# Kernel optimization log

Measured on AMD Instinct MI355X. Metric: run time of the kernel, lower is better.

The kernel has to match this reference:

```python
import jax, jax.numpy as jnp
import numpy as np
from functools import partial

NUM_ITERS = 3
NUM_CAPS = 8      # primary capsule count
NUM_CLASSES = 10
OUT_CH = 16       # digit capsule dim
INPUT_SIZE = 32 * 6 * 6  # 1152 primary capsule units per capsule map


def squash(s, axis=-1):
    # faithful to non_linear_squashing: s * (||s||^2/(1+||s||^2)) / (||s||+1e-10)
    norm_sqr = jnp.sum(s * s, axis=axis, keepdims=True)
    scale = jnp.sqrt(norm_sqr) + 1e-10
    mag = norm_sqr / (1.0 + norm_sqr)
    return s * mag / scale


def conv2d(x, w, b, stride):
    y = jax.lax.conv_general_dilated(
        x, w, window_strides=(stride, stride), padding='VALID',
        dimension_numbers=('NCHW', 'OIHW', 'NCHW'))
    return y + b[None, :, None, None]


def setup_inputs() -> dict:
    key = jax.random.key(0)
    ks = jax.random.split(key, 6)
    B = 256
    x = jax.random.normal(ks[0], (B, 1, 28, 28), dtype=jnp.float32)
    conv_w = jax.random.normal(ks[1], (256, 1, 9, 9), dtype=jnp.float32) * 0.05
    conv_b = jax.random.normal(ks[2], (256,), dtype=jnp.float32) * 0.05
    # 8 primary capsule conv units (256->32 each) fused into one 256->256 conv
    prim_w = jax.random.normal(ks[3], (NUM_CAPS * 32, 256, 9, 9), dtype=jnp.float32) * 0.02
    prim_b = jax.random.normal(ks[4], (NUM_CAPS * 32,), dtype=jnp.float32) * 0.02
    # digit routing weights (input_size, num_classes, out_channels, num_capsules)
    digit_w = jax.random.normal(ks[5], (INPUT_SIZE, NUM_CLASSES, OUT_CH, NUM_CAPS), dtype=jnp.float32)
    return {'x': x, 'conv_w': conv_w, 'conv_b': conv_b,
            'prim_w': prim_w, 'prim_b': prim_b, 'digit_w': digit_w}


def reference(x, conv_w, conv_b, prim_w, prim_b, digit_w):
    B = x.shape[0]
    # conv stack: 1->256 k9 s1 + ReLU  (28 -> 20); pool is MaxPool2d(1,1) = identity
    h = jax.nn.relu(conv2d(x, conv_w, conv_b, stride=1))  # (B,256,20,20)
    # primary capsules: 8 convs 256->32 k9 s2, no activation (nl_activation=False)
    p = conv2d(h, prim_w, prim_b, stride=2)               # (B,256,6,6)
    u = p.reshape(B, NUM_CAPS, -1)                        # (B,8,1152)
    u = squash(u, axis=-1)
    # digit layer with dynamic routing
    # u_i: (B, IS, 8);  u_j_i[b,i,c,o] = sum_k W[i,c,o,k] * u_i[b,i,k]
    u_i = jnp.transpose(u, (0, 2, 1))                     # (B,1152,8)
    u_j_i = jnp.einsum('icok,bik->bico', digit_w, u_i)    # (B,1152,10,16)
    b_ij = jnp.zeros((INPUT_SIZE, NUM_CLASSES), dtype=x.dtype)
    out = None
    for _ in range(NUM_ITERS):
        c_ij = jax.nn.softmax(b_ij, axis=0)               # softmax over input capsules (dim=1 in torch)
        s_j = jnp.einsum('ic,bico->bco', c_ij, u_j_i)     # (B,10,16)
        # original squashes (B,1,C,16,1) along dim=2 == the CLASS axis
        out = squash(s_j, axis=1)                         # (B,10,16)
        # agreement: mean over batch of <u_j_i, v_j>
        u_v = jnp.einsum('bico,bco->ic', u_j_i, out) / B  # (1152,10)
        b_ij = b_ij + u_v
    # torch returns out.squeeze(1) with shape (B, C, 16, 1)
    return out[..., None]
```

## Files before the change

kernel.cpp:

```cpp
#include <hip/hip_runtime.h>
#include <cstdint>
#include <cstddef>


typedef __attribute__((ext_vector_type(8))) short short8;
typedef __attribute__((ext_vector_type(4))) float f32x4;

#define PHALF 2359296

__device__ __forceinline__ unsigned short f2bf_rn(float x) {
    unsigned u = __float_as_uint(x);
    unsigned r = (u + 0x7fffu + ((u >> 16) & 1u)) >> 16;
    return (unsigned short)r;
}

__global__ void k_makew(const float* __restrict__ w2,
                        unsigned short* __restrict__ wt) {
    __shared__ float lw[20736];
    int ocg = blockIdx.x, icg = blockIdx.y, t = threadIdx.x;
    for (int idx = t; idx < 20736; idx += 256) {
        int row = idx / 81, k = idx % 81;
        int oc_l = row >> 5, ic_l = row & 31;
        lw[idx] = w2[((size_t)(ocg * 8 + oc_l) * 256 + icg * 32 + ic_l) * 81 + k];
    }
    __syncthreads();
    for (int idx = t; idx < 2592; idx += 256) {
        int k = idx >> 5;
        int r = idx & 31;
        int oc_l = r >> 2, sl = r & 3;
        unsigned short hi8[8];
        #pragma unroll
        for (int j = 0; j < 8; j++)
            hi8[j] = f2bf_rn(lw[(oc_l * 32 + sl * 8 + j) * 81 + k]);
        size_t o = ((size_t)(k * 256 + ocg * 8 + oc_l)) * 256 + icg * 32 + sl * 8;
        *(uint4*)&wt[o] = *(uint4*)hi8;
    }
}

__global__ void k_conv1(const float* __restrict__ x, const float* __restrict__ cw,
                        const float* __restrict__ cb,
                        unsigned short* __restrict__ h) {
    __shared__ float img[784];
    __shared__ float wsm[32 * 81];
    int b = blockIdx.x, ocg = blockIdx.y, t = threadIdx.x;
    for (int idx = t; idx < 784; idx += 256) img[idx] = x[b * 784 + idx];
    for (int idx = t; idx < 2592; idx += 256) wsm[idx] = cw[ocg * 2592 + idx];
    __syncthreads();
    int oc_l = t & 31, g = t >> 5;
    int oc = ocg * 32 + oc_l;
    float bias = cb[oc];
    const float* wp = &wsm[oc_l * 81];
    for (int q = g; q < 100; q += 8) {
        int py = q / 5, qx = (q % 5) * 4;
        float a0 = bias, a1 = bias, a2 = bias, a3 = bias;
        #pragma unroll
        for (int ky = 0; ky < 9; ky++) {
            const float* ir = &img[(py + ky) * 28 + qx];
            float r[12];
            #pragma unroll
            for (int j = 0; j < 12; j++) r[j] = ir[j];
            #pragma unroll
            for (int kx = 0; kx < 9; kx++) {
                float w = wp[ky * 9 + kx];
                a0 += r[kx] * w; a1 += r[kx + 1] * w;
                a2 += r[kx + 2] * w; a3 += r[kx + 3] * w;
            }
        }
        float v[4] = { fmaxf(a0, 0.f), fmaxf(a1, 0.f), fmaxf(a2, 0.f), fmaxf(a3, 0.f) };
        size_t base = ((size_t)b * 400 + py * 20 + qx) * 256 + oc;
        #pragma unroll
        for (int j = 0; j < 4; j++)
            h[base + (size_t)j * 256] = f2bf_rn(v[j]);
    }
}

__global__ __launch_bounds__(256) void k_conv2m(
    const unsigned short* __restrict__ h,
    const unsigned short* __restrict__ wt,
    float* __restrict__ pp)
{
    __shared__ unsigned short smem[24576];
    const int t = threadIdx.x;
    const int w = t >> 6, l = t & 63;
    const int mb = blockIdx.x, nb = blockIdx.y, z = blockIdx.z;

    const unsigned short* src;
    int nld, sbase;
    unsigned rowbase[16];
    if (w < 2) {
        src = h; nld = 16; sbase = w * 8192;
        #pragma unroll
        for (int ld = 0; ld < 16; ld++) {
            int row = ld * 8 + (l >> 3);
            int c = l & 7;
            int g = c ^ (row & 7);
            int P = mb * 128 + row;
            int b = P / 36, o = P % 36;
            int oy = o / 6, ox = o % 6;
            rowbase[ld] = (unsigned)((b * 400 + oy * 40 + ox * 2) * 256 + z * 128 + w * 64 + g * 8);
        }
    } else {
        int hh = w - 2;
        src = wt; nld = 8; sbase = 16384 + hh * 4096;
        #pragma unroll
        for (int ld = 0; ld < 8; ld++) {
            int oc = ld * 8 + (l >> 3);
            int c = l & 7;
            int g = c ^ (oc & 7);
            rowbase[ld] = (unsigned)((nb * 64 + oc) * 256 + z * 128 + hh * 64 + g * 8);
        }
    }

    const int wm = w & 1, wn = w >> 1;
    const int lane16 = l & 15, q = l >> 4;

    f32x4 acc[4][2] = {};

    for (int ky = 0; ky < 9; ky++) {
        for (int kx = 0; kx < 9; kx++) {
            const unsigned kofs = (w < 2) ? (unsigned)((ky * 20 + kx) * 256)
                                          : (unsigned)((ky * 9 + kx) * 65536);
            __syncthreads();
            for (int ld = 0; ld < nld; ld++) {
                __builtin_amdgcn_global_load_lds(
                    (const __attribute__((address_space(1))) unsigned int*)(const void*)(src + rowbase[ld] + kofs),
                    (__attribute__((address_space(3))) unsigned int*)(void*)(smem + sbase + ld * 512),
                    16, 0, 0);
            }
            __syncthreads();
            #pragma unroll
            for (int hh = 0; hh < 2; hh++) {
                #pragma unroll
                for (int ic2 = 0; ic2 < 2; ic2++) {
                    short8 a[4], b[2];
                    #pragma unroll
                    for (int mt = 0; mt < 4; mt++) {
                        int pixL = wm * 64 + mt * 16 + lane16;
                        int ps = (ic2 * 4 + q) ^ (pixL & 7);
                        a[mt] = *(const short8*)(smem + hh * 8192 + pixL * 64 + ps * 8);
                    }
                    #pragma unroll
                    for (int nt = 0; nt < 2; nt++) {
                        int ocL = wn * 32 + nt * 16 + lane16;
                        int ps = (ic2 * 4 + q) ^ (ocL & 7);
                        b[nt] = *(const short8*)(smem + 16384 + hh * 4096 + ocL * 64 + ps * 8);
                    }
                    #pragma unroll
                    for (int mt = 0; mt < 4; mt++)
                        #pragma unroll
                        for (int nt = 0; nt < 2; nt++)
                            acc[mt][nt] = __builtin_amdgcn_mfma_f32_16x16x32_bf16(a[mt], b[nt], acc[mt][nt], 0, 0, 0);
                }
            }
        }
    }

    float* pout = pp + (size_t)z * PHALF;
    #pragma unroll
    for (int mt = 0; mt < 4; mt++) {
        int pixG = mb * 128 + wm * 64 + mt * 16 + q * 4;
        int b = pixG / 36, p36 = pixG % 36;
        #pragma unroll
        for (int nt = 0; nt < 2; nt++) {
            int oc = nb * 64 + wn * 32 + nt * 16 + lane16;
            f32x4 v = acc[mt][nt];
            *(f32x4*)&pp[0] ;
            *(f32x4*)&pout[((size_t)(b * 256 + oc)) * 36 + p36] = v;
        }
    }
}

__global__ void k_squash1(const float* __restrict__ pp, const float* __restrict__ prim_b,
                          float* __restrict__ U) {
    __shared__ float red[4];
    int b = blockIdx.x >> 3, cap = blockIdx.x & 7;
    int t = threadIdx.x;
    const float* pa = pp + ((size_t)b * 256 + cap * 32) * 36;
    const float* pc = pa + PHALF;
    float v[5];
    float ss = 0.f;
    #pragma unroll
    for (int j = 0; j < 5; j++) {
        int idx = t + j * 256;
        if (idx < 1152) {
            int ch_l = idx / 36;
            float val = pa[idx] + pc[idx] + prim_b[cap * 32 + ch_l];
            v[j] = val; ss += val * val;
        } else v[j] = 0.f;
    }
    for (int off = 32; off; off >>= 1) ss += __shfl_down(ss, off);
    if ((t & 63) == 0) red[t >> 6] = ss;
    __syncthreads();
    float n2 = red[0] + red[1] + red[2] + red[3];
    float f = (n2 / (1.0f + n2)) / (sqrtf(n2) + 1e-10f);
    #pragma unroll
    for (int j = 0; j < 5; j++) {
        int idx = t + j * 256;
        if (idx < 1152) U[(size_t)b * 9216 + idx * 8 + cap] = v[j] * f;
    }
}

__global__ void k_dwt2(const float* __restrict__ dw, float* __restrict__ dwT2) {
    int co = blockIdx.x, t = threadIdx.x;
    int c = co >> 4, o = co & 15;
    const float* base = dw + c * 128 + o * 8;
    float* out = dwT2 + (size_t)co * 9216;
    for (int idx = t; idx < 9216; idx += 256) {
        int i = idx >> 3, k = idx & 7;
        out[idx] = base[(size_t)i * 1280 + k];
    }
}

__global__ void k_ut(const float* __restrict__ U, float* __restrict__ UT) {
    __shared__ float tl[64][65];
    int ikb = blockIdx.x, bb = blockIdx.y, t = threadIdx.x;
    for (int idx = t; idx < 1024; idx += 256) {
        int row = idx >> 4, c4 = idx & 15;
        float4 v = *(const float4*)&U[(size_t)(bb * 64 + row) * 9216 + ikb * 64 + c4 * 4];
        tl[c4 * 4 + 0][row] = v.x;
        tl[c4 * 4 + 1][row] = v.y;
        tl[c4 * 4 + 2][row] = v.z;
        tl[c4 * 4 + 3][row] = v.w;
    }
    __syncthreads();
    for (int idx = t; idx < 1024; idx += 256) {
        int row = idx >> 4, c4 = idx & 15;
        float4 v = make_float4(tl[row][c4 * 4 + 0], tl[row][c4 * 4 + 1],
                               tl[row][c4 * 4 + 2], tl[row][c4 * 4 + 3]);
        *(float4*)&UT[(size_t)(ikb * 64 + row) * 256 + bb * 64 + c4 * 4] = v;
    }
}

__global__ void k_softmax(const float* __restrict__ bij, float* __restrict__ csm) {
    __shared__ float red[4];
    int c = blockIdx.x, t = threadIdx.x;
    float vals[5];
    float mx = -1e30f;
    #pragma unroll
    for (int j = 0; j < 5; j++) {
        int i = t + j * 256;
        vals[j] = (i < 1152) ? bij[i * 10 + c] : -1e30f;
        mx = fmaxf(mx, vals[j]);
    }
    for (int off = 32; off; off >>= 1) mx = fmaxf(mx, __shfl_down(mx, off));
    if ((t & 63) == 0) red[t >> 6] = mx;
    __syncthreads();
    mx = fmaxf(fmaxf(red[0], red[1]), fmaxf(red[2], red[3]));
    __syncthreads();
    float s = 0.f;
    #pragma unroll
    for (int j = 0; j < 5; j++) {
        int i = t + j * 256;
        vals[j] = (i < 1152) ? expf(vals[j] - mx) : 0.f;
        s += vals[j];
    }
    for (int off = 32; off; off >>= 1) s += __shfl_down(s, off);
    if ((t & 63) == 0) red[t >> 6] = s;
    __syncthreads();
    s = red[0] + red[1] + red[2] + red[3];
    float inv = 1.0f / s;
    #pragma unroll
    for (int j = 0; j < 5; j++) {
        int i = t + j * 256;
        if (i < 1152) csm[i * 10 + c] = vals[j] * inv;
    }
}

__global__ __launch_bounds__(256) void k_gemm1(const float* __restrict__ U,
                                               const float* __restrict__ dwT2,
                                               const float* __restrict__ csm,
                                               float* __restrict__ part,
                                               int uniform) {
    __shared__ float Us[32 * 36];
    __shared__ float WsT[5120];
    __shared__ float cl[360];
    int mb = blockIdx.x, kc = blockIdx.y, t = threadIdx.x;
    int tc = t & 15, tb = t >> 4;
    if (!uniform)
        for (int idx = t; idx < 360; idx += 256) cl[idx] = csm[kc * 360 + idx];
    const float uscale = 1.0f / 1152.0f;
    float acc[2][10] = {};
    for (int ks = 0; ks < 9; ks++) {
        __syncthreads();
        {
            int bb = t >> 3, k4 = t & 7;
            *(float4*)&Us[bb * 36 + k4 * 4] =
                *(const float4*)&U[(size_t)(mb * 32 + bb) * 9216 + kc * 288 + ks * 32 + k4 * 4];
        }
        #pragma unroll
        for (int pass = 0; pass < 5; pass++) {
            int s = t + pass * 256;
            int co = s >> 3, p = s & 7;
            int kq = p ^ (co & 7);
            int ikl = ks * 32 + kq * 4;
            float4 v = *(const float4*)&dwT2[(size_t)co * 9216 + kc * 288 + ikl];
            float sc = uniform ? uscale : cl[(ikl >> 3) * 10 + (co >> 4)];
            v.x *= sc; v.y *= sc; v.z *= sc; v.w *= sc;
            *(float4*)&WsT[s * 4] = v;
        }
        __syncthreads();
        float a0[32], a1[32];
        #pragma unroll
        for (int kq = 0; kq < 8; kq++) {
            float4 v0 = *(const float4*)&Us[(tb * 2) * 36 + kq * 4];
            float4 v1 = *(const float4*)&Us[(tb * 2 + 1) * 36 + kq * 4];
            a0[kq * 4 + 0] = v0.x; a0[kq * 4 + 1] = v0.y; a0[kq * 4 + 2] = v0.z; a0[kq * 4 + 3] = v0.w;
            a1[kq * 4 + 0] = v1.x; a1[kq * 4 + 1] = v1.y; a1[kq * 4 + 2] = v1.z; a1[kq * 4 + 3] = v1.w;
        }
        #pragma unroll
        for (int j = 0; j < 10; j++) {
            int co = tc + 16 * j;
            int cx = co & 7, cbase = co * 32;
            #pragma unroll
            for (int kq = 0; kq < 8; kq++) {
                float4 wv = *(const float4*)&WsT[cbase + ((kq ^ cx) << 2)];
                acc[0][j] += a0[kq * 4 + 0] * wv.x; acc[0][j] += a0[kq * 4 + 1] * wv.y;
                acc[0][j] += a0[kq * 4 + 2] * wv.z; acc[0][j] += a0[kq * 4 + 3] * wv.w;
                acc[1][j] += a1[kq * 4 + 0] * wv.x; acc[1][j] += a1[kq * 4 + 1] * wv.y;
                acc[1][j] += a1[kq * 4 + 2] * wv.z; acc[1][j] += a1[kq * 4 + 3] * wv.w;
            }
        }
    }
    #pragma unroll
    for (int r = 0; r < 2; r++)
        #pragma unroll
        for (int j = 0; j < 10; j++)
            part[(size_t)kc * 40960 + (mb * 32 + tb * 2 + r) * 160 + tc + 16 * j] = acc[r][j];
}

__global__ void k_redsq(const float* __restrict__ part, float* __restrict__ out,
                        float* __restrict__ outT, int writeT) {
    __shared__ float sl[160];
    __shared__ float n2s[16];
    int b = blockIdx.x, t = threadIdx.x;
    float s = 0.f;
    if (t < 160) {
        for (int kc = 0; kc < 32; kc++) s += part[(size_t)kc * 40960 + b * 160 + t];
        sl[t] = s;
    }
    __syncthreads();
    if (t < 16) {
        float n2 = 0.f;
        #pragma unroll
        for (int c = 0; c < 10; c++) { float v = sl[c * 16 + t]; n2 += v * v; }
        n2s[t] = n2;
    }
    __syncthreads();
    if (t < 160) {
        float n2 = n2s[t & 15];
        float f = (n2 / (1.0f + n2)) / (sqrtf(n2) + 1e-10f);
        float r = s * f;
        out[(size_t)b * 160 + t] = r;
        if (writeT) outT[(size_t)t * 256 + b] = r;
    }
}

__global__ __launch_bounds__(256) void k_g2uv(const float* __restrict__ UT,
                                              const float* __restrict__ outTg,
                                              const float* __restrict__ dw,
                                              float* __restrict__ bij) {
    __shared__ float UsT[1024];
    __shared__ float OsT[5120];
    __shared__ float dwl[5120];
    __shared__ float sb[320];
    int blk = blockIdx.x, t = threadIdx.x;
    int tc = t & 15, tm = t >> 4;
    for (int idx = t; idx < 5120; idx += 256)
        dwl[idx] = dw[(size_t)blk * 5120 + idx];
    float acc[2][10] = {};
    for (int bs = 0; bs < 256; bs += 32) {
        __syncthreads();
        {
            int m = t >> 3, p = t & 7;
            int kq = p ^ (m & 7);
            *(float4*)&UsT[t * 4] =
                *(const float4*)&UT[(size_t)(blk * 32 + m) * 256 + bs + kq * 4];
        }
        #pragma unroll
        for (int pass = 0; pass < 5; pass++) {
            int s = t + pass * 256;
            int co = s >> 3, p = s & 7;
            int kq = p ^ (co & 7);
            *(float4*)&OsT[s * 4] =
                *(const float4*)&outTg[(size_t)co * 256 + bs + kq * 4];
        }
        __syncthreads();
        float a0[32], a1[32];
        int m0 = tm * 2, m1 = tm * 2 + 1;
        #pragma unroll
        for (int kq = 0; kq < 8; kq++) {
            float4 v0 = *(const float4*)&UsT[m0 * 32 + ((kq ^ (m0 & 7)) << 2)];
            float4 v1 = *(const float4*)&UsT[m1 * 32 + ((kq ^ (m1 & 7)) << 2)];
            a0[kq * 4 + 0] = v0.x; a0[kq * 4 + 1] = v0.y; a0[kq * 4 + 2] = v0.z; a0[kq * 4 + 3] = v0.w;
            a1[kq * 4 + 0] = v1.x; a1[kq * 4 + 1] = v1.y; a1[kq * 4 + 2] = v1.z; a1[kq * 4 + 3] = v1.w;
        }
        #pragma unroll
        for (int j = 0; j < 10; j++) {
            int co = tc + 16 * j;
            int cx = co & 7, cbase = co * 32;
            #pragma unroll
            for (int kq = 0; kq < 8; kq++) {
                float4 wv = *(const float4*)&OsT[cbase + ((kq ^ cx) << 2)];
                acc[0][j] += a0[kq * 4 + 0] * wv.x; acc[0][j] += a0[kq * 4 + 1] * wv.y;
                acc[0][j] += a0[kq * 4 + 2] * wv.z; acc[0][j] += a0[kq * 4 + 3] * wv.w;
                acc[1][j] += a1[kq * 4 + 0] * wv.x; acc[1][j] += a1[kq * 4 + 1] * wv.y;
                acc[1][j] += a1[kq * 4 + 2] * wv.z; acc[1][j] += a1[kq * 4 + 3] * wv.w;
            }
        }
    }
    #pragma unroll
    for (int r = 0; r < 2; r++) {
        int ik_l = tm * 2 + r;
        int i_l = ik_l >> 3, k = ik_l & 7;
        #pragma unroll
        for (int j = 0; j < 10; j++) {
            float v = acc[r][j] * dwl[i_l * 1280 + (j * 16 + tc) * 8 + k];
            v += __shfl_down(v, 8, 16);
            v += __shfl_down(v, 4, 16);
            v += __shfl_down(v, 2, 16);
            v += __shfl_down(v, 1, 16);
            if (tc == 0) sb[ik_l * 10 + j] = v;
        }
    }
    __syncthreads();
    if (t < 40) {
        int i_l = t / 10, c = t % 10;
        float s = 0.f;
        #pragma unroll
        for (int kk = 0; kk < 8; kk++) s += sb[(i_l * 8 + kk) * 10 + c];
        size_t o = (size_t)(blk * 4 + i_l) * 10 + c;
        bij[o] += s * (1.0f / 256.0f);
    }
}

extern "C" void kernel_launch(void* const* d_in, const int* in_sizes, int n_in,
                              void* d_out, int out_size, void* d_ws, size_t ws_size,
                              hipStream_t stream) {
    const float* x      = (const float*)d_in[0];
    const float* conv_w = (const float*)d_in[1];
    const float* conv_b = (const float*)d_in[2];
    const float* prim_w = (const float*)d_in[3];
    const float* prim_b = (const float*)d_in[4];
    const float* dw     = (const float*)d_in[5];

    char* wsb = (char*)d_ws;
    unsigned short* h  = (unsigned short*)(wsb);
    unsigned short* wt = (unsigned short*)(wsb + 52428800);
    float* pp   = (float*)(wsb + 63045632);
    float* U    = (float*)(wsb + 81920000);
    float* dwT2 = (float*)(wsb + 91357184);
    float* part = (float*)(wsb + 97255424);
    float* csm  = (float*)(wsb + 102498304);
    float* bij  = (float*)(wsb + 102544384);
    float* outT = (float*)(wsb + 102590464);
    float* outw = (float*)(wsb + 102754304);
    float* UT   = (float*)(wsb + 102918144);

    k_makew<<<dim3(32, 8), 256, 0, stream>>>(prim_w, wt);
    k_conv1<<<dim3(256, 8), 256, 0, stream>>>(x, conv_w, conv_b, h);
    k_dwt2<<<160, 256, 0, stream>>>(dw, dwT2);
    k_conv2m<<<dim3(72, 4, 2), 256, 0, stream>>>(h, wt, pp);
    k_squash1<<<2048, 256, 0, stream>>>(pp, prim_b, U);
    k_ut<<<dim3(144, 4), 256, 0, stream>>>(U, UT);
    hipMemsetAsync(bij, 0, 11520 * sizeof(float), stream);

    k_gemm1<<<dim3(8, 32), 256, 0, stream>>>(U, dwT2, csm, part, 1);
    k_redsq<<<256, 256, 0, stream>>>(part, outw, outT, 1);
    k_g2uv<<<288, 256, 0, stream>>>(UT, outT, dw, bij);
    k_softmax<<<10, 256, 0, stream>>>(bij, csm);
    k_gemm1<<<dim3(8, 32), 256, 0, stream>>>(U, dwT2, csm, part, 0);
    k_redsq<<<256, 256, 0, stream>>>(part, outw, outT, 1);
    k_g2uv<<<288, 256, 0, stream>>>(UT, outT, dw, bij);
    k_softmax<<<10, 256, 0, stream>>>(bij, csm);
    k_gemm1<<<dim3(8, 32), 256, 0, stream>>>(U, dwT2, csm, part, 0);
    k_redsq<<<256, 256, 0, stream>>>(part, (float*)d_out, outT, 0);
}
```

Measured before the change: 508.6 us.

## Retile primary-capsule conv into 96x128 tiles with four-way split-K partials

The primary conv GEMM changes from 128x64 tiles with split over two channel halves to 96x128 tiles. Work is split four ways: two channel halves times two ranges of kernel positions. Each block now loads 64 input channels per stage into a smaller shared-memory buffer and declares launch bounds for higher occupancy. Four partial outputs are written to workspace regions that alias later buffers (dwT2, UT), so k_dwt2 is moved after the squash kernel that sums the four partials. The change aims for better MFMA reuse per loaded tile and more blocks in flight, at the cost of twice as many barrier-separated load stages and extra partial-sum traffic.

Result: faster. 490.7 us (-3.5%).

```diff
diff --git a/kernel.cpp b/kernel.cpp
--- a/kernel.cpp
+++ b/kernel.cpp
@@ -74,52 +74,57 @@
     }
 }
 
-__global__ __launch_bounds__(256) void k_conv2m(
+__global__ __launch_bounds__(256, 4) void k_conv2m(
     const unsigned short* __restrict__ h,
     const unsigned short* __restrict__ wt,
-    float* __restrict__ pp)
+    float* __restrict__ p0, float* __restrict__ p1,
+    float* __restrict__ p2, float* __restrict__ p3)
 {
-    __shared__ unsigned short smem[24576];
+    __shared__ unsigned short smem[14336];
     const int t = threadIdx.x;
     const int w = t >> 6, l = t & 63;
-    const int mb = blockIdx.x, nb = blockIdx.y, z = blockIdx.z;
+    const int mb = blockIdx.x, nb = blockIdx.y, zz = blockIdx.z;
+    const int half = zz >> 1, seg = zz & 1;
 
     const unsigned short* src;
     int nld, sbase;
-    unsigned rowbase[16];
+    unsigned rowbase[8];
     if (w < 2) {
-        src = h; nld = 16; sbase = w * 8192;
-        #pragma unroll
-        for (int ld = 0; ld < 16; ld++) {
-            int row = ld * 8 + (l >> 3);
+        src = h; nld = 6; sbase = w * 3072;
+        #pragma unroll
+        for (int ld = 0; ld < 6; ld++) {
+            int row = w * 48 + ld * 8 + (l >> 3);
             int c = l & 7;
             int g = c ^ (row & 7);
-            int P = mb * 128 + row;
+            int P = mb * 96 + row;
             int b = P / 36, o = P % 36;
             int oy = o / 6, ox = o % 6;
-            rowbase[ld] = (unsigned)((b * 400 + oy * 40 + ox * 2) * 256 + z * 128 + w * 64 + g * 8);
+            rowbase[ld] = (unsigned)((b * 400 + oy * 40 + ox * 2) * 256 + half * 128 + g * 8);
         }
     } else {
-        int hh = w - 2;
-        src = wt; nld = 8; sbase = 16384 + hh * 4096;
+        src = wt; nld = 8; sbase = 6144 + (w - 2) * 4096;
         #pragma unroll
         for (int ld = 0; ld < 8; ld++) {
-            int oc = ld * 8 + (l >> 3);
+            int oc = (w - 2) * 64 + ld * 8 + (l >> 3);
             int c = l & 7;
             int g = c ^ (oc & 7);
-            rowbase[ld] = (unsigned)((nb * 64 + oc) * 256 + z * 128 + hh * 64 + g * 8);
+            rowbase[ld] = (unsigned)((nb * 128 + oc) * 256 + half * 128 + g * 8);
         }
     }
 
     const int wm = w & 1, wn = w >> 1;
     const int lane16 = l & 15, q = l >> 4;
 
-    f32x4 acc[4][2] = {};
-
-    for (int ky = 0; ky < 9; ky++) {
-        for (int kx = 0; kx < 9; kx++) {
-            const unsigned kofs = (w < 2) ? (unsigned)((ky * 20 + kx) * 256)
-                                          : (unsigned)((ky * 9 + kx) * 65536);
+    f32x4 acc[3][4] = {};
+
+    const int pos0 = seg ? 41 : 0;
+    const int pos1 = seg ? 81 : 41;
+    for (int pos = pos0; pos < pos1; ++pos) {
+        const int ky = pos / 9, kx = pos - ky * 9;
+        const unsigned kbase = (w < 2) ? (unsigned)((ky * 20 + kx) * 256)
+                                       : (unsigned)(pos * 65536);
+        for (int icc = 0; icc < 2; ++icc) {
+            const unsigned kofs = kbase + icc * 64;
             __syncthreads();
             for (int ld = 0; ld < nld; ld++) {
                 __builtin_amdgcn_global_load_lds(
@@ -129,54 +134,53 @@
             }
             __syncthreads();
             #pragma unroll
-            for (int hh = 0; hh < 2; hh++) {
+            for (int ic2 = 0; ic2 < 2; ic2++) {
+                short8 a[3], b[4];
                 #pragma unroll
-                for (int ic2 = 0; ic2 < 2; ic2++) {
-                    short8 a[4], b[2];
+                for (int mt = 0; mt < 3; mt++) {
+                    int pixL = wm * 48 + mt * 16 + lane16;
+                    int ps = (ic2 * 4 + q) ^ (pixL & 7);
+                    a[mt] = *(const short8*)(smem + pixL * 64 + ps * 8);
+                }
+                #pragma unroll
+                for (int nt = 0; nt < 4; nt++) {
+                    int ocL = wn * 64 + nt * 16 + lane16;
+                    int ps = (ic2 * 4 + q) ^ (ocL & 7);
+                    b[nt] = *(const short8*)(smem + 6144 + ocL * 64 + ps * 8);
+                }
+                #pragma unroll
+                for (int mt = 0; mt < 3; mt++)
                     #pragma unroll
-                    for (int mt = 0; mt < 4; mt++) {
-                        int pixL = wm * 64 + mt * 16 + lane16;
-                        int ps = (ic2 * 4 + q) ^ (pixL & 7);
-                        a[mt] = *(const short8*)(smem + hh * 8192 + pixL * 64 + ps * 8);
-                    }
-                    #pragma unroll
-                    for (int nt = 0; nt < 2; nt++) {
-                        int ocL = wn * 32 + nt * 16 + lane16;
-                        int ps = (ic2 * 4 + q) ^ (ocL & 7);
-                        b[nt] = *(const short8*)(smem + 16384 + hh * 4096 + ocL * 64 + ps * 8);
-                    }
-                    #pragma unroll
-                    for (int mt = 0; mt < 4; mt++)
-                        #pragma unroll
-                        for (int nt = 0; nt < 2; nt++)
-                            acc[mt][nt] = __builtin_amdgcn_mfma_f32_16x16x32_bf16(a[mt], b[nt], acc[mt][nt], 0, 0, 0);
-                }
+                    for (int nt = 0; nt < 4; nt++)
+                        acc[mt][nt] = __builtin_amdgcn_mfma_f32_16x16x32_bf16(a[mt], b[nt], acc[mt][nt], 0, 0, 0);
             }
         }
     }
 
-    float* pout = pp + (size_t)z * PHALF;
-    #pragma unroll
-    for (int mt = 0; mt < 4; mt++) {
-        int pixG = mb * 128 + wm * 64 + mt * 16 + q * 4;
+    float* pout = (zz == 0) ? p0 : (zz == 1) ? p1 : (zz == 2) ? p2 : p3;
+    #pragma unroll
+    for (int mt = 0; mt < 3; mt++) {
+        int pixG = mb * 96 + wm * 48 + mt * 16 + q * 4;
         int b = pixG / 36, p36 = pixG % 36;
         #pragma unroll
-        for (int nt = 0; nt < 2; nt++) {
-            int oc = nb * 64 + wn * 32 + nt * 16 + lane16;
-            f32x4 v = acc[mt][nt];
-            *(f32x4*)&pp[0] ;
-            *(f32x4*)&pout[((size_t)(b * 256 + oc)) * 36 + p36] = v;
-        }
-    }
-}
-
-__global__ void k_squash1(const float* __restrict__ pp, const float* __restrict__ prim_b,
-                          float* __restrict__ U) {
+        for (int nt = 0; nt < 4; nt++) {
+            int oc = nb * 128 + wn * 64 + nt * 16 + lane16;
+            *(f32x4*)&pout[((size_t)(b * 256 + oc)) * 36 + p36] = acc[mt][nt];
+        }
+    }
+}
+
+__global__ void k_squash1(const float* __restrict__ q0, const float* __restrict__ q1,
+                          const float* __restrict__ q2, const float* __restrict__ q3,
+                          const float* __restrict__ prim_b, float* __restrict__ U) {
     __shared__ float red[4];
     int b = blockIdx.x >> 3, cap = blockIdx.x & 7;
     int t = threadIdx.x;
-    const float* pa = pp + ((size_t)b * 256 + cap * 32) * 36;
-    const float* pc = pa + PHALF;
+    size_t base = ((size_t)b * 256 + cap * 32) * 36;
+    const float* pa = q0 + base;
+    const float* pb = q1 + base;
+    const float* pc = q2 + base;
+    const float* pd = q3 + base;
     float v[5];
     float ss = 0.f;
     #pragma unroll
@@ -184,7 +188,7 @@
         int idx = t + j * 256;
         if (idx < 1152) {
             int ch_l = idx / 36;
-            float val = pa[idx] + pc[idx] + prim_b[cap * 32 + ch_l];
+            float val = pa[idx] + pb[idx] + pc[idx] + pd[idx] + prim_b[cap * 32 + ch_l];
             v[j] = val; ss += val * val;
         } else v[j] = 0.f;
     }
@@ -446,21 +450,24 @@
     char* wsb = (char*)d_ws;
     unsigned short* h  = (unsigned short*)(wsb);
     unsigned short* wt = (unsigned short*)(wsb + 52428800);
-    float* pp   = (float*)(wsb + 63045632);
+    float* pp0  = (float*)(wsb + 63045632);
+    float* pp1  = (float*)(wsb + 72482816);
     float* U    = (float*)(wsb + 81920000);
     float* dwT2 = (float*)(wsb + 91357184);
+    float* pp3  = (float*)(wsb + 91357184);
     float* part = (float*)(wsb + 97255424);
     float* csm  = (float*)(wsb + 102498304);
     float* bij  = (float*)(wsb + 102544384);
     float* outT = (float*)(wsb + 102590464);
     float* outw = (float*)(wsb + 102754304);
     float* UT   = (float*)(wsb + 102918144);
+    float* pp2  = (float*)(wsb + 102918144);
 
     k_makew<<<dim3(32, 8), 256, 0, stream>>>(prim_w, wt);
     k_conv1<<<dim3(256, 8), 256, 0, stream>>>(x, conv_w, conv_b, h);
+    k_conv2m<<<dim3(96, 2, 4), 256, 0, stream>>>(h, wt, pp0, pp1, pp2, pp3);
+    k_squash1<<<2048, 256, 0, stream>>>(pp0, pp1, pp2, pp3, prim_b, U);
     k_dwt2<<<160, 256, 0, stream>>>(dw, dwT2);
-    k_conv2m<<<dim3(72, 4, 2), 256, 0, stream>>>(h, wt, pp);
-    k_squash1<<<2048, 256, 0, stream>>>(pp, prim_b, U);
     k_ut<<<dim3(144, 4), 256, 0, stream>>>(U, UT);
     hipMemsetAsync(bij, 0, 11520 * sizeof(float), stream);
 
```
